# Kernel optimization log

Measured on AMD Instinct MI355X. Metric: run time of the kernel, lower is better.

## Reference

```python
import jax, jax.numpy as jnp
import numpy as np

B, N, E = 64, 20000, 1280000

def setup_inputs() -> dict:
    key = jax.random.key(0)
    ks = jax.random.split(key, 7)
    x = jax.random.normal(ks[0], (B, N), dtype=jnp.float32)
    adj_values = jax.random.uniform(ks[1], (E,), dtype=jnp.float32)
    w = jax.random.normal(ks[2], (E,), dtype=jnp.float32)
    self_w = jax.random.normal(ks[3], (N,), dtype=jnp.float32)
    b = jax.random.normal(ks[4], (N,), dtype=jnp.float32)
    src = jax.random.randint(ks[5], (E,), 0, N, dtype=jnp.int32)
    dst = jax.random.randint(ks[6], (E,), 0, N, dtype=jnp.int32)
    return {"x": x, "adj_values": adj_values, "w": w, "self_w": self_w,
            "b": b, "src": src, "dst": dst}

def reference(x, adj_values, w, self_w, b, src, dst):
    # gather per-edge source-node features: [B, E]
    edge_vals = adj_values * x[:, src] * w
    # segment-sum over destination nodes (== sparse reduce_sum over source axis)
    # segment_sum reduces over the leading axis, so transpose to [E, B]
    ngh_sum = jax.ops.segment_sum(edge_vals.T, dst, num_segments=x.shape[1]).T  # [B, N]
    # NOTE: original module uses only inputs[0] for the self-loop (faithful quirk)
    self_loop = x[0] * self_w  # [N]
    out = ngh_sum * self_loop + b
    return jax.nn.relu(out)
```

## Files before the change

### kernel.cpp

```cpp
#include <hip/hip_runtime.h>

typedef unsigned long long u64;


#define GSZ   40
#define NG    500
#define CAP   4096
#define ETILE 2560
#define NBIN  512

__device__ __forceinline__ unsigned short f32_to_bf16(float f) {
    unsigned int u = __float_as_uint(f);
    u += 0x7FFFu + ((u >> 16) & 1u);
    return (unsigned short)(u >> 16);
}

__device__ __forceinline__ int wave_incl_scan(int v, int lane) {
#pragma unroll
    for (int d = 1; d < 64; d <<= 1) {
        int u = __shfl_up(v, d, 64);
        if (lane >= d) v += u;
    }
    return v;
}

__global__ __launch_bounds__(512) void scatter_kernel(
        const float* __restrict__ x, const float* __restrict__ adj,
        const float* __restrict__ w, const int* __restrict__ src,
        const int* __restrict__ dst, unsigned short* __restrict__ xTh,
        int* __restrict__ gcur, u64* __restrict__ packed, int N, int E) {
    __shared__ float tile[64][GSZ + 1];
    __shared__ u64 staged[ETILE];
    __shared__ unsigned short gof[ETILE];
    __shared__ int cnt[NBIN];
    __shared__ int ofs[NBIN];
    __shared__ int gbase[NBIN];
    __shared__ int wtot[8], wbase[8];
    int t = threadIdx.x, g = blockIdx.x;
    int lane = t & 63, wv = t >> 6;

    int n0 = g * GSZ;
    for (int lin = t; lin < 64 * GSZ; lin += 512) {
        int nl = lin % GSZ, b = lin / GSZ;
        int n = n0 + nl;
        tile[b][nl] = (n < N) ? x[(long)b * N + n] : 0.f;
    }
    cnt[t] = 0;
    __syncthreads();
    for (int lin = t; lin < 64 * GSZ; lin += 512) {
        int b = lin & 63, nl = lin >> 6;
        int n = n0 + nl;
        if (n < N) xTh[(long)n * 64 + b] = f32_to_bf16(tile[b][nl]);
    }

    int base = g * ETILE;
    u64 pk[5]; int gk[5]; int rk[5];
#pragma unroll
    for (int k = 0; k < 5; ++k) {
        int e = base + k * 512 + t;
        int gg; u64 p;
        if (e < E) {
            int d = dst[e];
            float c = adj[e] * w[e];
            gg = d / GSZ;
            p = ((u64)__float_as_uint(c) << 32)
              | (u64)(((unsigned int)src[e] << 6) | (unsigned int)(d - gg * GSZ));
        } else { gg = NBIN - 1; p = 0; }
        pk[k] = p; gk[k] = gg;
        rk[k] = atomicAdd(&cnt[gg], 1);
    }
    __syncthreads();

    int c = cnt[t];
    int incl = wave_incl_scan(c, lane);
    if (lane == 63) wtot[wv] = incl;
    __syncthreads();
    if (t == 0) {
        int run = 0;
#pragma unroll
        for (int k = 0; k < 8; ++k) { wbase[k] = run; run += wtot[k]; }
    }
    __syncthreads();
    ofs[t] = wbase[wv] + incl - c;
    if (t < NG && c > 0) gbase[t] = atomicAdd(&gcur[t], c);
    __syncthreads();

#pragma unroll
    for (int k = 0; k < 5; ++k) {
        int pos = ofs[gk[k]] + rk[k];
        staged[pos] = pk[k];
        gof[pos] = (unsigned short)gk[k];
    }
    __syncthreads();
#pragma unroll
    for (int k = 0; k < 5; ++k) {
        int i = k * 512 + t;
        int gg = gof[i];
        if (gg < NG) {
            int idx = gbase[gg] + (i - ofs[gg]);
            if (idx < CAP) packed[(long)gg * CAP + idx] = staged[i];
        }
    }
}

__global__ __launch_bounds__(1024) void sortreduce_kernel(
        const int* __restrict__ gcur, const u64* __restrict__ packed,
        const unsigned short* __restrict__ xTh, const float* __restrict__ x,
        const float* __restrict__ self_w, const float* __restrict__ bias,
        float* __restrict__ out, int N) {
    __shared__ u64 rec[CAP];
    __shared__ u64 rec2[CAP];
    __shared__ int hist[NBIN];
    __shared__ int hoff[NBIN + 1];
    __shared__ int cur[NBIN];
    __shared__ int wtot[8], wbase[8];
    int t = threadIdx.x, g = blockIdx.x;
    int lane = t & 63, wv = t >> 6;

    if (t < NBIN) hist[t] = 0;
    __syncthreads();
    long sbase = (long)g * CAP;
    int m = min(gcur[g], CAP);

    for (int i = t; i < m; i += 1024) {
        u64 p = packed[sbase + i];
        rec[i] = p;
        unsigned int lo = (unsigned int)p;
        int key = (int)((lo & 63u) << 3) | (int)((lo >> 6) >> 12);
        atomicAdd(&hist[key], 1);
    }
    __syncthreads();

    int c = (t < NBIN) ? hist[t] : 0;
    int incl = wave_incl_scan(c, lane);
    if (t < NBIN && lane == 63) wtot[wv] = incl;
    __syncthreads();
    if (t == 0) {
        int run = 0;
#pragma unroll
        for (int k = 0; k < 8; ++k) { wbase[k] = run; run += wtot[k]; }
        hoff[NBIN] = m;
    }
    __syncthreads();
    if (t < NBIN) {
        int ex = wbase[wv] + incl - c;
        hoff[t] = ex;
        cur[t] = ex;
    }
    __syncthreads();

    for (int i = t; i < m; i += 1024) {
        u64 p = rec[i];
        unsigned int lo = (unsigned int)p;
        int key = (int)((lo & 63u) << 3) | (int)((lo >> 6) >> 12);
        int pos = atomicAdd(&cur[key], 1);
        rec2[pos] = (p & 0xFFFFFFFF00000000ull) | (u64)(lo >> 6);
    }
    __syncthreads();

    float vals[3];
    int nvals = 0;
    for (int dl = wv; dl < GSZ; dl += 16) {
        int r0 = hoff[dl << 3];
        int r1 = hoff[(dl << 3) + 8];
        float a0 = 0.f, a1 = 0.f;
        int r = r0;
        for (; r + 8 <= r1; r += 8) {
            u64 p[8];
#pragma unroll
            for (int k = 0; k < 8; ++k) p[k] = rec2[r + k];
            float gg[8];
#pragma unroll
            for (int k = 0; k < 8; ++k) {
                int sk = (int)(unsigned int)p[k];
                float ck = __uint_as_float((unsigned int)(p[k] >> 32));
                float xv = __uint_as_float((unsigned int)xTh[sk * 64 + lane] << 16);
                gg[k] = ck * xv;
            }
            a0 += (gg[0] + gg[1]) + (gg[2] + gg[3]);
            a1 += (gg[4] + gg[5]) + (gg[6] + gg[7]);
        }
        for (; r < r1; ++r) {
            u64 p = rec2[r];
            int sk = (int)(unsigned int)p;
            float ck = __uint_as_float((unsigned int)(p >> 32));
            float xv = __uint_as_float((unsigned int)xTh[sk * 64 + lane] << 16);
            a0 += ck * xv;
        }
        vals[nvals++] = a0 + a1;
    }
    __syncthreads();

    float* sacc = (float*)rec;
    nvals = 0;
    for (int dl = wv; dl < GSZ; dl += 16)
        sacc[dl * 65 + lane] = vals[nvals++];
    __syncthreads();

    int nl = lane;
    int n = g * GSZ + nl;
    bool ok = (nl < GSZ) && (n < N);
    float sl = 0.f, bi = 0.f;
    if (ok) { sl = x[n] * self_w[n]; bi = bias[n]; }
#pragma unroll
    for (int i = 0; i < 4; ++i) {
        int b = wv * 4 + i;
        if (ok) {
            float v = sacc[nl * 65 + b] * sl + bi;
            out[(long)b * N + n] = fmaxf(v, 0.f);
        }
    }
}

extern "C" void kernel_launch(void* const* d_in, const int* in_sizes, int n_in,
                              void* d_out, int out_size, void* d_ws, size_t ws_size,
                              hipStream_t stream) {
    const float* x      = (const float*)d_in[0];
    const float* adj    = (const float*)d_in[1];
    const float* w      = (const float*)d_in[2];
    const float* self_w = (const float*)d_in[3];
    const float* bias   = (const float*)d_in[4];
    const int*   src    = (const int*)d_in[5];
    const int*   dst    = (const int*)d_in[6];

    int N = in_sizes[3];
    int E = in_sizes[1];
    (void)n_in; (void)ws_size; (void)out_size;

    u64*            packed = (u64*)d_ws;
    unsigned short* xTh    = (unsigned short*)(packed + (size_t)NG * CAP);
    int*            gcur   = (int*)(xTh + (size_t)N * 64);
    float*          out    = (float*)d_out;

    hipMemsetAsync((void*)gcur, 0, NG * sizeof(int), stream);
    hipLaunchKernelGGL(scatter_kernel, dim3(NG), dim3(512), 0, stream,
                       x, adj, w, src, dst, xTh, gcur, packed, N, E);
    hipLaunchKernelGGL(sortreduce_kernel, dim3(NG), dim3(1024), 0, stream,
                       gcur, packed, xTh, x, self_w, bias, out, N);
}
```

Measured before the change: 119.2 us.

## Replace global atomic bucket scatter with per-block sorted runs and offset table

The scatter kernel now writes its locally bucket-sorted edge tile contiguously and stores per-block bucket offsets, instead of using global atomics to scatter records into per-group buckets. The reduce kernel reads each source block's run for its group through a binary search over prefix offsets, builds the histogram while loading, and drops the staging copy and the memset. This removes global atomics and scattered writes, and it changes the write and read access pattern. The trade-off is gathers from 500 separate segments, a per-element binary search, and a transposed goff read. The inner scan also relies on rpos[NBIN-1] covering all NG entries, which holds only because NG is less than NBIN.

```diff
diff --git a/kernel.cpp b/kernel.cpp
--- a/kernel.cpp
+++ b/kernel.cpp
@@ -28,13 +28,11 @@
         const float* __restrict__ x, const float* __restrict__ adj,
         const float* __restrict__ w, const int* __restrict__ src,
         const int* __restrict__ dst, unsigned short* __restrict__ xTh,
-        int* __restrict__ gcur, u64* __restrict__ packed, int N, int E) {
+        int* __restrict__ goff, u64* __restrict__ packed, int N, int E) {
     __shared__ float tile[64][GSZ + 1];
     __shared__ u64 staged[ETILE];
-    __shared__ unsigned short gof[ETILE];
     __shared__ int cnt[NBIN];
     __shared__ int ofs[NBIN];
-    __shared__ int gbase[NBIN];
     __shared__ int wtot[8], wbase[8];
     int t = threadIdx.x, g = blockIdx.x;
     int lane = t & 63, wv = t >> 6;
@@ -82,56 +80,44 @@
     }
     __syncthreads();
     ofs[t] = wbase[wv] + incl - c;
-    if (t < NG && c > 0) gbase[t] = atomicAdd(&gcur[t], c);
     __syncthreads();
 
 #pragma unroll
     for (int k = 0; k < 5; ++k) {
         int pos = ofs[gk[k]] + rk[k];
         staged[pos] = pk[k];
-        gof[pos] = (unsigned short)gk[k];
-    }
-    __syncthreads();
-#pragma unroll
-    for (int k = 0; k < 5; ++k) {
-        int i = k * 512 + t;
-        int gg = gof[i];
-        if (gg < NG) {
-            int idx = gbase[gg] + (i - ofs[gg]);
-            if (idx < CAP) packed[(long)gg * CAP + idx] = staged[i];
-        }
-    }
+    }
+    goff[g * NBIN + t] = ofs[t];
+    __syncthreads();
+    long obase = (long)g * ETILE;
+#pragma unroll
+    for (int k = 0; k < 5; ++k)
+        packed[obase + k * 512 + t] = staged[k * 512 + t];
 }
 
 __global__ __launch_bounds__(1024) void sortreduce_kernel(
-        const int* __restrict__ gcur, const u64* __restrict__ packed,
+        const u64* __restrict__ packed, const int* __restrict__ goff,
         const unsigned short* __restrict__ xTh, const float* __restrict__ x,
         const float* __restrict__ self_w, const float* __restrict__ bias,
         float* __restrict__ out, int N) {
-    __shared__ u64 rec[CAP];
     __shared__ u64 rec2[CAP];
+    __shared__ float sacc[GSZ * 65];
+    __shared__ int rstart[NG];
+    __shared__ int rpos[NBIN];
     __shared__ int hist[NBIN];
     __shared__ int hoff[NBIN + 1];
-    __shared__ int cur[NBIN];
     __shared__ int wtot[8], wbase[8];
     int t = threadIdx.x, g = blockIdx.x;
     int lane = t & 63, wv = t >> 6;
 
     if (t < NBIN) hist[t] = 0;
-    __syncthreads();
-    long sbase = (long)g * CAP;
-    int m = min(gcur[g], CAP);
-
-    for (int i = t; i < m; i += 1024) {
-        u64 p = packed[sbase + i];
-        rec[i] = p;
-        unsigned int lo = (unsigned int)p;
-        int key = (int)((lo & 63u) << 3) | (int)((lo >> 6) >> 12);
-        atomicAdd(&hist[key], 1);
-    }
-    __syncthreads();
-
-    int c = (t < NBIN) ? hist[t] : 0;
+    int c = 0;
+    if (t < NG) {
+        int s0 = goff[t * NBIN + g];
+        int s1 = goff[t * NBIN + g + 1];
+        rstart[t] = s0;
+        c = s1 - s0;
+    }
     int incl = wave_incl_scan(c, lane);
     if (t < NBIN && lane == 63) wtot[wv] = incl;
     __syncthreads();
@@ -139,27 +125,58 @@
         int run = 0;
 #pragma unroll
         for (int k = 0; k < 8; ++k) { wbase[k] = run; run += wtot[k]; }
+    }
+    __syncthreads();
+    if (t < NBIN) rpos[t] = wbase[wv] + incl - c;
+    __syncthreads();
+    int m = min(rpos[NBIN - 1], CAP);
+
+    u64 pv[4]; int rk4[4];
+#pragma unroll
+    for (int k = 0; k < 4; ++k) {
+        int i = (k << 10) + t;
+        pv[k] = 0; rk4[k] = -1;
+        if (i < m) {
+            int lo = 0;
+#pragma unroll
+            for (int s = 256; s >= 1; s >>= 1) {
+                int j = lo + s;
+                if (j < NG && rpos[j] <= i) lo = j;
+            }
+            u64 p = packed[(long)lo * ETILE + rstart[lo] + (i - rpos[lo])];
+            pv[k] = p;
+            unsigned int lo32 = (unsigned int)p;
+            int key = (int)((lo32 & 63u) << 3) | (int)(lo32 >> 18);
+            rk4[k] = atomicAdd(&hist[key], 1);
+        }
+    }
+    __syncthreads();
+
+    c = (t < NBIN) ? hist[t] : 0;
+    incl = wave_incl_scan(c, lane);
+    if (t < NBIN && lane == 63) wtot[wv] = incl;
+    __syncthreads();
+    if (t == 0) {
+        int run = 0;
+#pragma unroll
+        for (int k = 0; k < 8; ++k) { wbase[k] = run; run += wtot[k]; }
         hoff[NBIN] = m;
     }
     __syncthreads();
-    if (t < NBIN) {
-        int ex = wbase[wv] + incl - c;
-        hoff[t] = ex;
-        cur[t] = ex;
-    }
-    __syncthreads();
-
-    for (int i = t; i < m; i += 1024) {
-        u64 p = rec[i];
-        unsigned int lo = (unsigned int)p;
-        int key = (int)((lo & 63u) << 3) | (int)((lo >> 6) >> 12);
-        int pos = atomicAdd(&cur[key], 1);
-        rec2[pos] = (p & 0xFFFFFFFF00000000ull) | (u64)(lo >> 6);
-    }
-    __syncthreads();
-
-    float vals[3];
-    int nvals = 0;
+    if (t < NBIN) hoff[t] = wbase[wv] + incl - c;
+    __syncthreads();
+
+#pragma unroll
+    for (int k = 0; k < 4; ++k) {
+        if (rk4[k] >= 0) {
+            u64 p = pv[k];
+            unsigned int lo32 = (unsigned int)p;
+            int key = (int)((lo32 & 63u) << 3) | (int)(lo32 >> 18);
+            rec2[hoff[key] + rk4[k]] = (p & 0xFFFFFFFF00000000ull) | (u64)(lo32 >> 6);
+        }
+    }
+    __syncthreads();
+
     for (int dl = wv; dl < GSZ; dl += 16) {
         int r0 = hoff[dl << 3];
         int r1 = hoff[(dl << 3) + 8];
@@ -187,14 +204,8 @@
             float xv = __uint_as_float((unsigned int)xTh[sk * 64 + lane] << 16);
             a0 += ck * xv;
         }
-        vals[nvals++] = a0 + a1;
-    }
-    __syncthreads();
-
-    float* sacc = (float*)rec;
-    nvals = 0;
-    for (int dl = wv; dl < GSZ; dl += 16)
-        sacc[dl * 65 + lane] = vals[nvals++];
+        sacc[dl * 65 + lane] = a0 + a1;
+    }
     __syncthreads();
 
     int nl = lane;
@@ -228,13 +239,12 @@
     (void)n_in; (void)ws_size; (void)out_size;
 
     u64*            packed = (u64*)d_ws;
-    unsigned short* xTh    = (unsigned short*)(packed + (size_t)NG * CAP);
-    int*            gcur   = (int*)(xTh + (size_t)N * 64);
+    unsigned short* xTh    = (unsigned short*)(packed + (size_t)NG * ETILE);
+    int*            goff   = (int*)(xTh + (size_t)N * 64);
     float*          out    = (float*)d_out;
 
-    hipMemsetAsync((void*)gcur, 0, NG * sizeof(int), stream);
     hipLaunchKernelGGL(scatter_kernel, dim3(NG), dim3(512), 0, stream,
-                       x, adj, w, src, dst, xTh, gcur, packed, N, E);
+                       x, adj, w, src, dst, xTh, goff, packed, N, E);
     hipLaunchKernelGGL(sortreduce_kernel, dim3(NG), dim3(1024), 0, stream,
-                       gcur, packed, xTh, x, self_w, bias, out, N);
-}
+                       packed, goff, xTh, x, self_w, bias, out, N);
+}
```

After: 113.0 us. 5.2% less time.
